# Kernel optimization log

Hardware: AMD Instinct MI355X
Metric: run time of the kernel (lower is better)

The kernel has to match this reference:

```python
import jax, jax.numpy as jnp
import numpy as np

B, N, NB, E, H, A, K, D = 32, 512, 10, 1024, 256, 82, 4, 3


def setup_inputs() -> dict:
    key = jax.random.key(0)
    ks = iter(jax.random.split(key, 64))
    f = lambda shape: jax.random.normal(next(ks), shape, jnp.float32) * 0.05
    inp = {
        "atom_fea": jax.random.normal(next(ks), (B, N, A), jnp.float32),
        "bond_fea": jax.random.normal(next(ks), (B, E, 6), jnp.float32),
        "d_anb": jax.random.randint(next(ks), (B, N, NB), 0, N),
        "d_bnb": jax.random.randint(next(ks), (B, N, NB), 0, E),
        "d_nbs_mask": (jax.random.uniform(next(ks), (B, N, NB)) < 0.8).astype(jnp.float32),
        "d_mask": (jax.random.uniform(next(ks), (B, N)) < 0.9).astype(jnp.float32),
        "Wv": f((A, H)), "bv": f((H,)),
        "Wa_main": f((D, K, H, H)), "ba_main": f((D, K, H)),
        "Wa_super": f((D, K, H, H)), "ba_super": f((D, K, H)),
        "Wm": f((D, K, H, H)), "bm": f((D, K, H)),
        "Wbmm": f((D, K, H)), "bbmm": f((D, K)),
        "Wm2s": f((D, K * H, H)), "bm2s": f((D, H)),
        "Ws2m": f((D, H, H)), "bs2m": f((D, H)),
        "Wsup": f((D, H, H)), "bsup": f((D, H)),
        "Wzm1": f((D, H, H)), "bzm1": f((D, H)),
        "Wzm2": f((D, H, H)), "bzm2": f((D, H)),
        "Wzs1": f((D, H, H)), "bzs1": f((D, H)),
        "Wzs2": f((D, H, H)), "bzs2": f((D, H)),
        "Wu2": f((D, H + 6, H)), "bu2": f((D, H)),
        "Wu1": f((D, 2 * H, H)), "bu1": f((D, H)),
    }
    return inp


def mask_softmax(a, mask):
    a_max = jnp.max(a, -1, keepdims=True)
    e = jnp.exp(a - a_max) * mask
    return e / (jnp.sum(e, -1, keepdims=True) + 1e-6)


def _forward(atom_fea, bond_fea, d_nbs_mask, d_mask,
             Wv, bv, Wa_main, ba_main, Wa_super, ba_super, Wm, bm, Wbmm, bbmm,
             Wm2s, bm2s, Ws2m, bs2m, Wsup, bsup,
             Wzm1, bzm1, Wzm2, bzm2, Wzs1, bzs1, Wzs2, bzs2,
             Wu2, bu2, Wu1, bu1, d_anb, d_bnb):
    Bn = atom_fea.shape[0]
    bidx = jnp.arange(Bn)[:, None, None]
    # vertex embedding (default leaky_relu slope 0.01)
    vf = jax.nn.leaky_relu(atom_fea @ Wv + bv, 0.01)            # [B,N,H]
    sf = jnp.sum(vf * d_mask[:, :, None], axis=1, keepdims=True)  # [B,1,H]
    mask3 = d_nbs_mask[..., None]                               # [B,N,NB,1]
    for d in range(D):
        # --- multi-head main->super attention (vectorized over heads k) ---
        a_main = jnp.tanh(jnp.einsum('bnh,khj->bknj', vf, Wa_main[d]) + ba_main[d][None, :, None, :])
        a_super = jnp.tanh(jnp.einsum('boh,khj->bkoj', sf, Wa_super[d]) + ba_super[d][None, :, None, :])
        a = jnp.einsum('bknh,kh->bkn', a_main * a_super, Wbmm[d]) + bbmm[d][None, :, None]
        attn = mask_softmax(a, d_mask[:, None, :])               # [B,K,N]
        mvf = jnp.einsum('bnh,khj->bknj', vf, Wm[d]) + bm[d][None, :, None, :]
        m2s = jnp.einsum('bkn,bknh->bkh', attn, mvf).reshape(Bn, 1, K * H)
        main_to_super = jnp.tanh(m2s @ Wm2s[d] + bm2s[d])        # [B,1,H]
        # --- wln unit: gather neighbors, MLP, masked sum (slope 0.1) ---
        vnei = vf[bidx, d_anb]                                   # [B,N,NB,H]
        enei = bond_fea[bidx, d_bnb]                             # [B,N,NB,6]
        lnei = jnp.concatenate([vnei, enei], -1)                 # [B,N,NB,H+6]
        nei = jax.nn.leaky_relu(lnei @ Wu2[d] + bu2[d], 0.1)
        nei = jnp.sum(nei * mask3, axis=2)                       # [B,N,H]
        main_self = jax.nn.leaky_relu(jnp.concatenate([vf, nei], -1) @ Wu1[d] + bu1[d], 0.1)
        # --- GRU-style gated updates ---
        super_to_main = jnp.tanh(sf @ Ws2m[d] + bs2m[d])         # [B,1,H]
        super_self = jnp.tanh(sf @ Wsup[d] + bsup[d])            # [B,1,H]
        z_main = jax.nn.sigmoid(main_self @ Wzm1[d] + bzm1[d] + super_to_main @ Wzm2[d] + bzm2[d])
        vf = (1 - z_main) * main_self + z_main * super_to_main
        z_sup = jax.nn.sigmoid(super_self @ Wzs1[d] + bzs1[d] + main_to_super @ Wzs2[d] + bzs2[d])
        sf = (1 - z_sup) * super_self + z_sup * main_to_super    # [B,1,H]; sum over dim 1 is a no-op
    return vf, sf


def reference(atom_fea, bond_fea, d_anb, d_bnb, d_nbs_mask, d_mask,
              Wv, bv, Wa_main, ba_main, Wa_super, ba_super, Wm, bm, Wbmm, bbmm,
              Wm2s, bm2s, Ws2m, bs2m, Wsup, bsup,
              Wzm1, bzm1, Wzm2, bzm2, Wzs1, bzs1, Wzs2, bzs2,
              Wu2, bu2, Wu1, bu1):
    return _forward(atom_fea, bond_fea, d_nbs_mask, d_mask,
                    Wv, bv, Wa_main, ba_main, Wa_super, ba_super, Wm, bm, Wbmm, bbmm,
                    Wm2s, bm2s, Ws2m, bs2m, Wsup, bsup,
                    Wzm1, bzm1, Wzm2, bzm2, Wzs1, bzs1, Wzs2, bzs2,
                    Wu2, bu2, Wu1, bu1, d_anb, d_bnb)
```

## Files before the change

### kernel.cpp

```cpp
#include <hip/hip_runtime.h>
#include <hip/hip_bf16.h>

#define B_ 32
#define N_ 512
#define NB_ 10
#define E_ 1024
#define H_ 256
#define A_ 82
#define K_ 4
#define D_ 3
#define M_ (B_*N_)

typedef unsigned short u16;
typedef __attribute__((ext_vector_type(8))) short bf16x8;
typedef __attribute__((ext_vector_type(4))) float f32x4;

__device__ __forceinline__ float b2f(u16 u){
    unsigned int x = ((unsigned int)u) << 16;
    return __builtin_bit_cast(float, x);
}
__device__ __forceinline__ u16 f2b(float f){
    unsigned int x = __builtin_bit_cast(unsigned int, f);
    unsigned int lsb = (x >> 16) & 1u;
    x += 0x7fffu + lsb;
    return (u16)(x >> 16);
}
__device__ __forceinline__ float sigmoidf_(float x){ return 1.f/(1.f+expf(-x)); }

static constexpr int CVT_N[31] = {
    B_*E_*6, B_*N_*NB_, B_*N_,
    A_*H_, H_,
    D_*K_*H_*H_, D_*K_*H_, D_*K_*H_*H_, D_*K_*H_,
    D_*K_*H_*H_, D_*K_*H_, D_*K_*H_, D_*K_,
    D_*K_*H_*H_, D_*H_, D_*H_*H_, D_*H_,
    D_*H_*H_, D_*H_, D_*H_*H_, D_*H_,
    D_*H_*H_, D_*H_, D_*H_*H_, D_*H_,
    D_*H_*H_, D_*H_, D_*(H_+6)*H_, D_*H_,
    D_*2*H_*H_, D_*H_
};
struct Offs { long v[32]; };
static constexpr Offs mk_offs(){
    Offs o{}; o.v[0]=0;
    for(int i=0;i<31;i++) o.v[i+1]=o.v[i]+CVT_N[i];
    return o;
}
static constexpr Offs CVT_OFF = mk_offs();

struct Ptrs { const void* p[31]; };

__global__ void k_detect(const unsigned short* __restrict__ wv_raw, int* __restrict__ flag){
    float v = b2f(wv_raw[threadIdx.x]);
    bool plaus = (v==v) && (fabsf(v) < 100.0f);
    unsigned long long m = __ballot(plaus);
    if (threadIdx.x==0) *flag = (m == ~0ULL) ? 1 : 0;
}

__global__ void k_cvt(Ptrs ptrs, float* __restrict__ dst, const int* __restrict__ flag){
    int t = blockIdx.y;
    int n = CVT_N[t];
    int i4 = blockIdx.x*256 + threadIdx.x;
    if (i4*4 >= n) return;
    const void* src = ptrs.p[t];
    float4 o;
    if (*flag){
        ushort4 u = ((const ushort4*)src)[i4];
        o.x=b2f(u.x); o.y=b2f(u.y); o.z=b2f(u.z); o.w=b2f(u.w);
    } else {
        o = ((const float4*)src)[i4];
    }
    *(float4*)(dst + CVT_OFF.v[t] + (size_t)i4*4) = o;
}

__global__ void k_wt(const float* __restrict__ Wam, const float* __restrict__ Wu2,
                     const float* __restrict__ Wu1, const float* __restrict__ Wzm1,
                     u16* __restrict__ WT){
    int mi = blockIdx.z;
    const float* src;
    if (mi<12)      src = Wam  + (size_t)mi*H_*H_;
    else if (mi<15) src = Wu2  + (size_t)(mi-12)*(H_+6)*H_;
    else if (mi<18) src = Wu1  + (size_t)(mi-15)*2*H_*H_;
    else if (mi<21) src = Wu1  + (size_t)(mi-18)*2*H_*H_ + (size_t)H_*H_;
    else            src = Wzm1 + (size_t)(mi-21)*H_*H_;
    __shared__ float t[32][33];
    int x = threadIdx.x, y = threadIdx.y;
    int k0 = blockIdx.y*32, n0 = blockIdx.x*32;
    for(int yy=y; yy<32; yy+=8) t[yy][x] = src[(size_t)(k0+yy)*H_ + n0+x];
    __syncthreads();
    u16* dst = WT + ((size_t)mi*8 + (k0>>5))*(256*32);
    for(int yy=y; yy<32; yy+=8) dst[(size_t)(n0+yy)*32 + x] = f2b(t[x][yy]);
}

__global__ void k_embed(const u16* __restrict__ atom, const float* __restrict__ Wv,
                        const float* __restrict__ bv, float* __restrict__ vf,
                        u16* __restrict__ vf_bf, const int* __restrict__ flag){
    __shared__ float arow[8][A_];
    int r0 = blockIdx.x*8; int j = threadIdx.x;
    int fl = *flag;
    for(int i=j;i<8*A_;i+=256){
        int r=i/A_, a=i-r*A_;
        arow[r][a] = fl ? b2f(atom[(size_t)(r0+r)*A_+a])
                        : ((const float*)atom)[(size_t)(r0+r)*A_+a];
    }
    __syncthreads();
    float acc[8];
    float bj = bv[j];
    #pragma unroll
    for(int r=0;r<8;r++) acc[r]=bj;
    for(int a=0;a<A_;a++){
        float w = Wv[a*H_+j];
        #pragma unroll
        for(int r=0;r<8;r++) acc[r] += arow[r][a]*w;
    }
    #pragma unroll
    for(int r=0;r<8;r++){
        float v = acc[r];
        v = v>0.f ? v : 0.01f*v;
        vf[(size_t)(r0+r)*H_+j] = v;
        vf_bf[(size_t)(r0+r)*H_+j] = f2b(v);
    }
}

__global__ void k_sf0(const float* __restrict__ vf, const float* __restrict__ dmask,
                      float* __restrict__ sf){
    int b = blockIdx.x, h = threadIdx.x;
    __shared__ float mk[N_];
    for(int n=threadIdx.x;n<N_;n+=256) mk[n] = dmask[b*N_+n];
    __syncthreads();
    float s=0.f;
    #pragma unroll 8
    for(int n=0;n<N_;n++) s += mk[n]*vf[((size_t)b*N_+n)*H_ + h];
    sf[b*H_+h]=s;
}

__global__ void k_s1(int d, const float* __restrict__ sf,
    const float* __restrict__ Was, const float* __restrict__ bas,
    const float* __restrict__ Wbmm,
    const float* __restrict__ Ws2m, const float* __restrict__ bs2m,
    const float* __restrict__ Wsup, const float* __restrict__ bsup,
    float* __restrict__ asw, float* __restrict__ s2m, float* __restrict__ ssf)
{
    int b = blockIdx.x, m = blockIdx.y, j = threadIdx.x;
    __shared__ float sfl[H_];
    sfl[j] = sf[b*H_+j];
    __syncthreads();
    const float* W; float bias;
    if (m < 4){ W = Was + (size_t)(d*K_+m)*H_*H_; bias = bas[(d*K_+m)*H_+j]; }
    else if (m==4){ W = Ws2m + (size_t)d*H_*H_; bias = bs2m[d*H_+j]; }
    else { W = Wsup + (size_t)d*H_*H_; bias = bsup[d*H_+j]; }
    float acc = bias;
    #pragma unroll 8
    for(int h=0;h<H_;h++) acc += sfl[h]*W[h*H_+j];
    float v = tanhf(acc);
    if (m < 4) asw[(b*K_+m)*H_+j] = v * Wbmm[(d*K_+m)*H_+j];
    else if (m==4) s2m[b*H_+j] = v;
    else ssf[b*H_+j] = v;
}

__global__ void k_s2(int d, const float* __restrict__ s2m,
    const float* __restrict__ Wzm2, const float* __restrict__ bzm2,
    float* __restrict__ stm2p)
{
    int b=blockIdx.x, c=blockIdx.y, j=threadIdx.x;
    __shared__ float xl[64];
    if (j<64) xl[j] = s2m[b*H_ + c*64 + j];
    __syncthreads();
    const float* W = Wzm2 + (size_t)d*H_*H_ + (size_t)(c*64)*H_;
    float acc = (c==0) ? bzm2[d*H_+j] : 0.f;
    #pragma unroll 8
    for(int h=0;h<64;h++) acc += xl[h]*W[h*H_+j];
    stm2p[((size_t)c*B_+b)*H_+j] = acc;
}

__device__ __forceinline__ void gemm_rf(const u16* __restrict__ Abf,
                                        const u16* __restrict__ WTg,
                                        f32x4 acc[2][8])
{
    int tid = threadIdx.x;
    int lane = tid & 63, wave = tid >> 6;
    int wy = wave >> 1, wx = wave & 1;
    int quad = lane >> 4, l15 = lane & 15;
    const u16* aP0 = Abf + (size_t)(wy*32 + l15)*H_ + quad*8;
    const u16* aP1 = aP0 + 16*H_;
    const u16* wP  = WTg + (size_t)(wx*128 + l15)*32 + quad*8;
    #pragma unroll
    for(int mt=0;mt<2;mt++)
        #pragma unroll
        for(int nt=0;nt<8;nt++) acc[mt][nt]=(f32x4){0.f,0.f,0.f,0.f};
    bf16x8 a0[2],a1[2],w0[8],w1[8];
    a0[0]=*(const bf16x8*)(aP0); a0[1]=*(const bf16x8*)(aP1);
    #pragma unroll
    for(int nt=0;nt<8;nt++) w0[nt]=*(const bf16x8*)(wP + nt*512);

#define GLOAD(AN,WN,K0) \
    AN[0]=*(const bf16x8*)(aP0 + (K0)); AN[1]=*(const bf16x8*)(aP1 + (K0)); \
    _Pragma("unroll") for(int nt=0;nt<8;nt++) WN[nt]=*(const bf16x8*)(wP + (size_t)((K0)>>5)*8192 + nt*512);
#define GMMA(AC,WC) \
    _Pragma("unroll") for(int mt=0;mt<2;mt++) \
    _Pragma("unroll") for(int nt=0;nt<8;nt++) \
        acc[mt][nt]=__builtin_amdgcn_mfma_f32_16x16x32_bf16(AC[mt],WC[nt],acc[mt][nt],0,0,0);

    GLOAD(a1,w1,32);  GMMA(a0,w0);
    GLOAD(a0,w0,64);  GMMA(a1,w1);
    GLOAD(a1,w1,96);  GMMA(a0,w0);
    GLOAD(a0,w0,128); GMMA(a1,w1);
    GLOAD(a1,w1,160); GMMA(a0,w0);
    GLOAD(a0,w0,192); GMMA(a1,w1);
    GLOAD(a1,w1,224); GMMA(a0,w0);
    GMMA(a1,w1);
#undef GLOAD
#undef GMMA
}

__global__ __launch_bounds__(256,3) void k_gemm_big(int d, const u16* __restrict__ vf_bf,
    const u16* __restrict__ WT, const float* __restrict__ ba_main,
    const float* __restrict__ bbmm, const float* __restrict__ bu1,
    const float* __restrict__ asw, float* __restrict__ score,
    float* __restrict__ proj_u2, float* __restrict__ pu1a)
{
    __shared__ float sred[64*33];
    int m0 = blockIdx.x*64;
    int seg = blockIdx.y;
    int b = m0 >> 9;
    int mi;
    if (seg < 4)      mi = d*4+seg;
    else if (seg==4)  mi = 12+d;
    else              mi = 15+d;
    f32x4 acc[2][8];
    gemm_rf(vf_bf + (size_t)m0*H_, WT + (size_t)mi*H_*H_, acc);
    int tid=threadIdx.x, lane=tid&63, wave=tid>>6;
    int wy=wave>>1, wx=wave&1, quad=lane>>4, l15=lane&15;
    if (seg < 4){
        const float* aswp = asw + (size_t)(b*K_+seg)*H_;
        const float* bap  = ba_main + (size_t)(d*K_+seg)*H_;
        float bbv[8], awv[8];
        #pragma unroll
        for(int nt=0;nt<8;nt++){
            int col = wx*128+nt*16+l15;
            bbv[nt]=bap[col]; awv[nt]=aswp[col];
        }
        #pragma unroll
        for(int mt=0;mt<2;mt++)
            #pragma unroll
            for(int r=0;r<4;r++){
                float p=0.f;
                #pragma unroll
                for(int nt=0;nt<8;nt++)
                    p += tanhf(acc[mt][nt][r]+bbv[nt])*awv[nt];
                int row = wy*32+mt*16+quad*4+r;
                sred[row*33 + wx*16+l15] = p;
            }
        __syncthreads();
        if (tid < 64){
            float s=0.f;
            #pragma unroll 8
            for(int i=0;i<32;i++) s += sred[tid*33+i];
            score[(size_t)(b*K_+seg)*N_ + (m0&511) + tid] = s + bbmm[d*K_+seg];
        }
    } else if (seg==4){
        #pragma unroll
        for(int mt=0;mt<2;mt++)
            #pragma unroll
            for(int nt=0;nt<8;nt++){
                int col = wx*128+nt*16+l15;
                #pragma unroll
                for(int r=0;r<4;r++){
                    int row = m0 + wy*32+mt*16+quad*4+r;
                    proj_u2[(size_t)row*H_+col] = acc[mt][nt][r];
                }
            }
    } else {
        const float* bp = bu1 + d*H_;
        #pragma unroll
        for(int mt=0;mt<2;mt++)
            #pragma unroll
            for(int nt=0;nt<8;nt++){
                int col = wx*128+nt*16+l15;
                float bb = bp[col];
                #pragma unroll
                for(int r=0;r<4;r++){
                    int row = m0 + wy*32+mt*16+quad*4+r;
                    pu1a[(size_t)row*H_+col] = acc[mt][nt][r] + bb;
                }
            }
    }
}

__global__ __launch_bounds__(256,3) void k_mainself(int d, u16* __restrict__ neims,
    const u16* __restrict__ WT, float* __restrict__ pu)
{
    int m0 = blockIdx.x*64;
    f32x4 acc[2][8];
    gemm_rf(neims + (size_t)m0*H_, WT + (size_t)(18+d)*H_*H_, acc);
    __syncthreads();
    int tid=threadIdx.x, lane=tid&63, wave=tid>>6;
    int wy=wave>>1, wx=wave&1, quad=lane>>4, l15=lane&15;
    #pragma unroll
    for(int mt=0;mt<2;mt++)
        #pragma unroll
        for(int nt=0;nt<8;nt++){
            int col = wx*128+nt*16+l15;
            #pragma unroll
            for(int r=0;r<4;r++){
                int row = m0 + wy*32+mt*16+quad*4+r;
                float v = acc[mt][nt][r] + pu[(size_t)row*H_+col];
                v = v>0.f? v : 0.1f*v;
                pu[(size_t)row*H_+col] = v;
                neims[(size_t)row*H_+col] = f2b(v);
            }
        }
}

__global__ __launch_bounds__(256,3) void k_update(int d, const float* __restrict__ ms,
    const u16* __restrict__ ms_bf, const u16* __restrict__ WT, const float* __restrict__ bzm1,
    const float* __restrict__ stm2p, const float* __restrict__ s2m,
    float* __restrict__ vf, u16* __restrict__ vf_bf)
{
    int m0 = blockIdx.x*64; int b = m0>>9;
    f32x4 acc[2][8];
    gemm_rf(ms_bf + (size_t)m0*H_, WT + (size_t)(21+d)*H_*H_, acc);
    int tid=threadIdx.x, lane=tid&63, wave=tid>>6;
    int wy=wave>>1, wx=wave&1, quad=lane>>4, l15=lane&15;
    #pragma unroll
    for(int mt=0;mt<2;mt++)
        #pragma unroll
        for(int nt=0;nt<8;nt++){
            int col = wx*128+nt*16+l15;
            float bz = bzm1[d*H_+col];
            float st = stm2p[(size_t)(0*B_+b)*H_+col] + stm2p[(size_t)(1*B_+b)*H_+col]
                     + stm2p[(size_t)(2*B_+b)*H_+col] + stm2p[(size_t)(3*B_+b)*H_+col];
            float sm = s2m[b*H_+col];
            #pragma unroll
            for(int r=0;r<4;r++){
                int row = m0 + wy*32+mt*16+quad*4+r;
                float z = sigmoidf_(acc[mt][nt][r] + bz + st);
                float msv = ms[(size_t)row*H_+col];
                float o = (1.f-z)*msv + z*sm;
                vf[(size_t)row*H_+col] = o;
                vf_bf[(size_t)row*H_+col] = f2b(o);
            }
        }
}

__global__ void k_softmax(float* __restrict__ score, const float* __restrict__ dmask,
                          float* __restrict__ sumattn){
    int b = blockIdx.x, k = blockIdx.y;
    int tid = threadIdx.x;
    __shared__ float sh[256];
    float* a = score + (size_t)(b*K_+k)*N_;
    float v0 = a[tid], v1 = a[tid+256];
    sh[tid]=fmaxf(v0,v1); __syncthreads();
    for(int s=128;s>0;s>>=1){ if(tid<s) sh[tid]=fmaxf(sh[tid],sh[tid+s]); __syncthreads(); }
    float m = sh[0]; __syncthreads();
    float e0 = expf(v0-m)*dmask[b*N_+tid], e1 = expf(v1-m)*dmask[b*N_+tid+256];
    sh[tid]=e0+e1; __syncthreads();
    for(int s=128;s>0;s>>=1){ if(tid<s) sh[tid]+=sh[tid+s]; __syncthreads(); }
    float S = sh[0];
    float inv = 1.f/(S+1e-6f);
    a[tid]=e0*inv; a[tid+256]=e1*inv;
    if(tid==0) sumattn[b*K_+k]=S*inv;
}

__global__ void k_t2(const float* __restrict__ attn, const float* __restrict__ vf,
                     float* __restrict__ tpart){
    int b=blockIdx.x, k=blockIdx.y, c=blockIdx.z, h=threadIdx.x;
    __shared__ float at[256];
    at[h] = attn[(size_t)(b*K_+k)*N_ + c*256 + h];
    __syncthreads();
    float acc=0.f;
    const float* vfp = vf + ((size_t)b*N_ + c*256)*H_ + h;
    #pragma unroll 8
    for(int n=0;n<256;n++) acc += at[n]*vfp[(size_t)n*H_];
    tpart[((size_t)(c*B_+b)*K_+k)*H_+h]=acc;
}

__global__ void k_m1(int d, const float* __restrict__ tpart, const float* __restrict__ sumattn,
    const float* __restrict__ Wm, const float* __restrict__ bm, float* __restrict__ m2s)
{
    int b=blockIdx.x, k=blockIdx.y, j=threadIdx.x;
    __shared__ float tl[H_];
    tl[j] = tpart[((size_t)(0*B_+b)*K_+k)*H_+j] + tpart[((size_t)(1*B_+b)*K_+k)*H_+j];
    __syncthreads();
    const float* W = Wm + (size_t)(d*K_+k)*H_*H_;
    float acc = sumattn[b*K_+k]*bm[(d*K_+k)*H_+j];
    #pragma unroll 8
    for(int h=0;h<H_;h++) acc += tl[h]*W[h*H_+j];
    m2s[(size_t)(b*K_+k)*H_+j]=acc;
}

__global__ void k_m2(int d, const float* __restrict__ m2s, const float* __restrict__ Wm2s,
                     float* __restrict__ mtsp)
{
    int b=blockIdx.x, c=blockIdx.y, j=threadIdx.x;
    __shared__ float xl[H_];
    xl[j]=m2s[(size_t)(b*K_+c)*H_+j];
    __syncthreads();
    const float* W = Wm2s + (size_t)d*(K_*H_)*H_ + (size_t)(c*H_)*H_;
    float acc=0.f;
    #pragma unroll 8
    for(int h=0;h<H_;h++) acc += xl[h]*W[h*H_+j];
    mtsp[((size_t)c*B_+b)*H_+j]=acc;
}

__global__ void k_mts(int d, const float* __restrict__ mtsp, const float* __restrict__ bm2s,
                      float* __restrict__ mts){
    int b=blockIdx.x, j=threadIdx.x;
    float acc = bm2s[d*H_+j];
    #pragma unroll
    for(int c=0;c<4;c++) acc += mtsp[((size_t)c*B_+b)*H_+j];
    mts[b*H_+j]=tanhf(acc);
}

__global__ void k_m3(int d, const float* __restrict__ ssf, const float* __restrict__ mts,
    const float* __restrict__ Wzs1, const float* __restrict__ Wzs2,
    float* __restrict__ p1, float* __restrict__ p2)
{
    int b=blockIdx.x, m=blockIdx.y, j=threadIdx.x;
    __shared__ float xl[H_];
    const float* x = m ? mts : ssf;
    xl[j]=x[b*H_+j];
    __syncthreads();
    const float* W = (m ? Wzs2 : Wzs1) + (size_t)d*H_*H_;
    float acc=0.f;
    #pragma unroll 8
    for(int h=0;h<H_;h++) acc += xl[h]*W[h*H_+j];
    (m ? p2 : p1)[b*H_+j]=acc;
}

__global__ void k_sfup(int d, const float* __restrict__ p1, const float* __restrict__ p2,
    const float* __restrict__ bzs1, const float* __restrict__ bzs2,
    const float* __restrict__ ssf, const float* __restrict__ mts, float* __restrict__ sf)
{
    int b=blockIdx.x, j=threadIdx.x;
    float z = sigmoidf_(p1[b*H_+j]+bzs1[d*H_+j]+p2[b*H_+j]+bzs2[d*H_+j]);
    sf[b*H_+j]=(1.f-z)*ssf[b*H_+j]+z*mts[b*H_+j];
}

__global__ void k_nei(int d, const int* __restrict__ anb, const int* __restrict__ bnb,
    const float* __restrict__ nbm, const float* __restrict__ bond,
    const float* __restrict__ Wu2, const float* __restrict__ bu2,
    const float* __restrict__ proj_u2, u16* __restrict__ nei_bf)
{
    __shared__ float W2s[6][256];
    __shared__ float bfeat[4][NB_][6];
    __shared__ int ai[4][NB_]; __shared__ int bi[4][NB_]; __shared__ float mk[4][NB_];
    int r0 = blockIdx.x*4; int b = r0 >> 9; int h = threadIdx.x;
    const float* W2 = Wu2 + (size_t)d*(H_+6)*H_ + (size_t)H_*H_;
    for(int i=h;i<6*H_;i+=256) W2s[i>>8][i&255] = W2[i];
    if (h < 4*NB_){
        int r=h/NB_, jn=h-r*NB_;
        ai[r][jn]=anb[(size_t)(r0+r)*NB_+jn];
        bi[r][jn]=bnb[(size_t)(r0+r)*NB_+jn];
        mk[r][jn]=nbm[(size_t)(r0+r)*NB_+jn];
    }
    __syncthreads();
    if (h < 4*NB_*6){
        int r=h/(NB_*6), rem=h-r*(NB_*6), jn=rem/6, i=rem-jn*6;
        bfeat[r][jn][i]=bond[((size_t)b*E_+bi[r][jn])*6+i];
    }
    __syncthreads();
    float bu = bu2[d*H_+h];
    #pragma unroll
    for(int r=0;r<4;r++){
        float acc=0.f;
        #pragma unroll
        for(int jn=0;jn<NB_;jn++){
            float v = proj_u2[((size_t)b*N_+ai[r][jn])*H_+h] + bu;
            #pragma unroll
            for(int i=0;i<6;i++) v += bfeat[r][jn][i]*W2s[i][h];
            v = v>0.f? v : 0.1f*v;
            acc += mk[r][jn]*v;
        }
        nei_bf[(size_t)(r0+r)*H_+h]=f2b(acc);
    }
}

__global__ void k_out(const float* __restrict__ vf, const float* __restrict__ sf,
                      void* __restrict__ out, const int* __restrict__ flag){
    int idx = blockIdx.x*256 + threadIdx.x;
    const int total = M_*H_ + B_*H_;
    if (idx >= total) return;
    float v = (idx < M_*H_) ? vf[idx] : sf[idx - M_*H_];
    if (*flag) ((unsigned short*)out)[idx] = f2b(v);
    else       ((float*)out)[idx] = v;
}

extern "C" void kernel_launch(void* const* d_in, const int* in_sizes, int n_in,
                              void* d_out, int out_size, void* d_ws, size_t ws_size,
                              hipStream_t stream)
{
    const int* anb = (const int*)d_in[2];
    const int* bnb = (const int*)d_in[3];

    float* ws   = (float*)d_ws;
    int*   flag = (int*)ws;
    float* cvt  = ws + 64;
    float* p    = cvt + ((CVT_OFF.v[31] + 63) & ~63L);
    float* vf        = p; p += (size_t)M_*H_;
    float* proj_u2   = p; p += (size_t)M_*H_;
    float* proj_u1a  = p; p += (size_t)M_*H_;
    u16*   vf_bf     = (u16*)p; p += (size_t)M_*H_/2;
    u16*   neims     = (u16*)p; p += (size_t)M_*H_/2;
    float* sf        = p; p += B_*H_;
    float* score     = p; p += B_*K_*N_;
    float* sumattn   = p; p += B_*K_;
    float* asw       = p; p += B_*K_*H_;
    float* s2m       = p; p += B_*H_;
    float* ssf       = p; p += B_*H_;
    float* stm2p     = p; p += 4*B_*H_;
    float* tpart     = p; p += 2*B_*K_*H_;
    float* m2s       = p; p += B_*K_*H_;
    float* mtsp      = p; p += 4*B_*H_;
    float* mts       = p; p += B_*H_;
    float* p1        = p; p += B_*H_;
    float* p2        = p; p += B_*H_;
    u16*   WT        = (u16*)p;

    const float* cBond = cvt + CVT_OFF.v[0];
    const float* cNbm  = cvt + CVT_OFF.v[1];
    const float* cDm   = cvt + CVT_OFF.v[2];
    const float* cWv   = cvt + CVT_OFF.v[3];
    const float* cbv   = cvt + CVT_OFF.v[4];
    const float* cWam  = cvt + CVT_OFF.v[5];
    const float* cbam  = cvt + CVT_OFF.v[6];
    const float* cWas  = cvt + CVT_OFF.v[7];
    const float* cbas  = cvt + CVT_OFF.v[8];
    const float* cWm   = cvt + CVT_OFF.v[9];
    const float* cbm   = cvt + CVT_OFF.v[10];
    const float* cWbmm = cvt + CVT_OFF.v[11];
    const float* cbbmm = cvt + CVT_OFF.v[12];
    const float* cWm2s = cvt + CVT_OFF.v[13];
    const float* cbm2s = cvt + CVT_OFF.v[14];
    const float* cWs2m = cvt + CVT_OFF.v[15];
    const float* cbs2m = cvt + CVT_OFF.v[16];
    const float* cWsup = cvt + CVT_OFF.v[17];
    const float* cbsup = cvt + CVT_OFF.v[18];
    const float* cWzm1 = cvt + CVT_OFF.v[19];
    const float* cbzm1 = cvt + CVT_OFF.v[20];
    const float* cWzm2 = cvt + CVT_OFF.v[21];
    const float* cbzm2 = cvt + CVT_OFF.v[22];
    const float* cWzs1 = cvt + CVT_OFF.v[23];
    const float* cbzs1 = cvt + CVT_OFF.v[24];
    const float* cWzs2 = cvt + CVT_OFF.v[25];
    const float* cbzs2 = cvt + CVT_OFF.v[26];
    const float* cWu2  = cvt + CVT_OFF.v[27];
    const float* cbu2  = cvt + CVT_OFF.v[28];
    const float* cWu1  = cvt + CVT_OFF.v[29];
    const float* cbu1  = cvt + CVT_OFF.v[30];

    Ptrs ptrs;
    {
        int idx[31] = {1,4,5,6,7,8,9,10,11,12,13,14,15,16,17,18,19,20,21,
                       22,23,24,25,26,27,28,29,30,31,32,33};
        for(int i=0;i<31;i++) ptrs.p[i] = d_in[idx[i]];
    }

    k_detect<<<1,64,0,stream>>>((const unsigned short*)d_in[6], flag);
    {
        int maxv4 = (D_*K_*H_*H_ + 3)/4;
        int gx = (maxv4 + 255)/256;
        k_cvt<<<dim3(gx,31),256,0,stream>>>(ptrs, cvt, flag);
    }
    k_wt<<<dim3(8,8,24),dim3(32,8),0,stream>>>(cWam, cWu2, cWu1, cWzm1, WT);

    k_embed<<<M_/8,256,0,stream>>>((const u16*)d_in[0], cWv, cbv, vf, vf_bf, flag);
    k_sf0<<<B_,256,0,stream>>>(vf, cDm, sf);
    for(int d=0; d<D_; d++){
        k_s1<<<dim3(B_,6),256,0,stream>>>(d, sf, cWas, cbas, cWbmm,
                                          cWs2m, cbs2m, cWsup, cbsup, asw, s2m, ssf);
        k_s2<<<dim3(B_,4),256,0,stream>>>(d, s2m, cWzm2, cbzm2, stm2p);
        k_gemm_big<<<dim3(M_/64,6),256,0,stream>>>(d, vf_bf, WT, cbam, cbbmm, cbu1,
                                                   asw, score, proj_u2, proj_u1a);
        k_softmax<<<dim3(B_,K_),256,0,stream>>>(score, cDm, sumattn);
        k_t2<<<dim3(B_,K_,2),256,0,stream>>>(score, vf, tpart);
        k_m1<<<dim3(B_,K_),256,0,stream>>>(d, tpart, sumattn, cWm, cbm, m2s);
        k_m2<<<dim3(B_,4),256,0,stream>>>(d, m2s, cWm2s, mtsp);
        k_mts<<<B_,256,0,stream>>>(d, mtsp, cbm2s, mts);
        k_m3<<<dim3(B_,2),256,0,stream>>>(d, ssf, mts, cWzs1, cWzs2, p1, p2);
        k_sfup<<<B_,256,0,stream>>>(d, p1, p2, cbzs1, cbzs2, ssf, mts, sf);
        k_nei<<<M_/4,256,0,stream>>>(d, anb, bnb, cNbm, cBond, cWu2, cbu2, proj_u2, neims);
        k_mainself<<<M_/64,256,0,stream>>>(d, neims, WT, proj_u1a);
        k_update<<<M_/64,256,0,stream>>>(d, proj_u1a, neims, WT, cbzm1, stm2p, s2m, vf, vf_bf);
    }
    k_out<<<(M_*H_+B_*H_+255)/256,256,0,stream>>>(vf, sf, d_out, flag);
}
```

Before: 766.4 us.

## Stage weight tiles into LDS via async global_load_lds double buffering

Before, each wave loaded its weight fragments straight from global memory into registers. Now each 32-wide K slice of the weight matrix is staged into a double-buffered LDS tile with global_load_lds, and the weight transpose kernel writes a fragment-ordered layout that matches this. The aim is to share weight loads across the four waves of a block and overlap the next slice's fetch with the current MFMAs. In exchange it adds a barrier per K step and 32KB of LDS per block, which may cut occupancy below the launch-bounds target of 3 blocks.

After: 725.4 us. -5.3%, faster.

```diff
diff --git a/kernel.cpp b/kernel.cpp
--- a/kernel.cpp
+++ b/kernel.cpp
@@ -86,8 +86,12 @@
     int k0 = blockIdx.y*32, n0 = blockIdx.x*32;
     for(int yy=y; yy<32; yy+=8) t[yy][x] = src[(size_t)(k0+yy)*H_ + n0+x];
     __syncthreads();
-    u16* dst = WT + ((size_t)mi*8 + (k0>>5))*(256*32);
-    for(int yy=y; yy<32; yy+=8) dst[(size_t)(n0+yy)*32 + x] = f2b(t[x][yy]);
+    u16* dst = WT + ((size_t)mi*8 + (k0>>5))*8192;
+    int quad = x>>3, j = x&7;
+    for(int yy=y; yy<32; yy+=8){
+        int n = n0+yy, nt = n>>4, lv = n&15;
+        dst[nt*512 + quad*128 + lv*8 + j] = f2b(t[x][yy]);
+    }
 }
 
 __global__ void k_embed(const u16* __restrict__ atom, const float* __restrict__ Wv,
@@ -171,9 +175,21 @@
     stm2p[((size_t)c*B_+b)*H_+j] = acc;
 }
 
-__device__ __forceinline__ void gemm_rf(const u16* __restrict__ Abf,
-                                        const u16* __restrict__ WTg,
-                                        f32x4 acc[2][8])
+__device__ __forceinline__ void stageW(const u16* __restrict__ g, u16* l){
+    int t = threadIdx.x;
+    const u16* gs = g + t*8;
+    u16* ls = l + t*8;
+    #pragma unroll
+    for(int it=0; it<4; ++it)
+        __builtin_amdgcn_global_load_lds(
+            (const __attribute__((address_space(1))) void*)(gs + it*2048),
+            (__attribute__((address_space(3))) void*)(ls + it*2048),
+            16, 0, 0);
+}
+
+__device__ __forceinline__ void gemm_ldsW(const u16* __restrict__ Abf,
+                                          const u16* __restrict__ WTg,
+                                          u16* Wlds, f32x4 acc[2][8])
 {
     int tid = threadIdx.x;
     int lane = tid & 63, wave = tid >> 6;
@@ -181,34 +197,38 @@
     int quad = lane >> 4, l15 = lane & 15;
     const u16* aP0 = Abf + (size_t)(wy*32 + l15)*H_ + quad*8;
     const u16* aP1 = aP0 + 16*H_;
-    const u16* wP  = WTg + (size_t)(wx*128 + l15)*32 + quad*8;
+    bf16x8 a[4][2];
+    #pragma unroll
+    for(int s=0;s<3;s++){
+        a[s][0] = *(const bf16x8*)(aP0 + s*32);
+        a[s][1] = *(const bf16x8*)(aP1 + s*32);
+    }
+    stageW(WTg, Wlds);
     #pragma unroll
     for(int mt=0;mt<2;mt++)
         #pragma unroll
         for(int nt=0;nt<8;nt++) acc[mt][nt]=(f32x4){0.f,0.f,0.f,0.f};
-    bf16x8 a0[2],a1[2],w0[8],w1[8];
-    a0[0]=*(const bf16x8*)(aP0); a0[1]=*(const bf16x8*)(aP1);
-    #pragma unroll
-    for(int nt=0;nt<8;nt++) w0[nt]=*(const bf16x8*)(wP + nt*512);
-
-#define GLOAD(AN,WN,K0) \
-    AN[0]=*(const bf16x8*)(aP0 + (K0)); AN[1]=*(const bf16x8*)(aP1 + (K0)); \
-    _Pragma("unroll") for(int nt=0;nt<8;nt++) WN[nt]=*(const bf16x8*)(wP + (size_t)((K0)>>5)*8192 + nt*512);
-#define GMMA(AC,WC) \
-    _Pragma("unroll") for(int mt=0;mt<2;mt++) \
-    _Pragma("unroll") for(int nt=0;nt<8;nt++) \
-        acc[mt][nt]=__builtin_amdgcn_mfma_f32_16x16x32_bf16(AC[mt],WC[nt],acc[mt][nt],0,0,0);
-
-    GLOAD(a1,w1,32);  GMMA(a0,w0);
-    GLOAD(a0,w0,64);  GMMA(a1,w1);
-    GLOAD(a1,w1,96);  GMMA(a0,w0);
-    GLOAD(a0,w0,128); GMMA(a1,w1);
-    GLOAD(a1,w1,160); GMMA(a0,w0);
-    GLOAD(a0,w0,192); GMMA(a1,w1);
-    GLOAD(a1,w1,224); GMMA(a0,w0);
-    GMMA(a1,w1);
-#undef GLOAD
-#undef GMMA
+    __syncthreads();
+    #pragma unroll
+    for(int s=0;s<8;s++){
+        if (s<7) stageW(WTg + (size_t)(s+1)*8192, Wlds + ((s+1)&1)*8192);
+        if (s<5){
+            int sl = s+3;
+            a[sl&3][0] = *(const bf16x8*)(aP0 + sl*32);
+            a[sl&3][1] = *(const bf16x8*)(aP1 + sl*32);
+        }
+        const u16* wb = Wlds + (s&1)*8192 + wx*4096 + quad*128 + l15*8;
+        bf16x8 w[8];
+        #pragma unroll
+        for(int nt=0;nt<8;nt++) w[nt] = *(const bf16x8*)(wb + nt*512);
+        #pragma unroll
+        for(int mt=0;mt<2;mt++)
+            #pragma unroll
+            for(int nt=0;nt<8;nt++)
+                acc[mt][nt] = __builtin_amdgcn_mfma_f32_16x16x32_bf16(
+                    a[s&3][mt], w[nt], acc[mt][nt], 0,0,0);
+        __syncthreads();
+    }
 }
 
 __global__ __launch_bounds__(256,3) void k_gemm_big(int d, const u16* __restrict__ vf_bf,
@@ -217,7 +237,7 @@
     const float* __restrict__ asw, float* __restrict__ score,
     float* __restrict__ proj_u2, float* __restrict__ pu1a)
 {
-    __shared__ float sred[64*33];
+    __shared__ __attribute__((aligned(16))) u16 Wlds[2*8192];
     int m0 = blockIdx.x*64;
     int seg = blockIdx.y;
     int b = m0 >> 9;
@@ -226,10 +246,11 @@
     else if (seg==4)  mi = 12+d;
     else              mi = 15+d;
     f32x4 acc[2][8];
-    gemm_rf(vf_bf + (size_t)m0*H_, WT + (size_t)mi*H_*H_, acc);
+    gemm_ldsW(vf_bf + (size_t)m0*H_, WT + (size_t)mi*H_*H_, Wlds, acc);
     int tid=threadIdx.x, lane=tid&63, wave=tid>>6;
     int wy=wave>>1, wx=wave&1, quad=lane>>4, l15=lane&15;
     if (seg < 4){
+        float* sred = (float*)Wlds;
         const float* aswp = asw + (size_t)(b*K_+seg)*H_;
         const float* bap  = ba_main + (size_t)(d*K_+seg)*H_;
         float bbv[8], awv[8];
@@ -288,10 +309,10 @@
 __global__ __launch_bounds__(256,3) void k_mainself(int d, u16* __restrict__ neims,
     const u16* __restrict__ WT, float* __restrict__ pu)
 {
+    __shared__ __attribute__((aligned(16))) u16 Wlds[2*8192];
     int m0 = blockIdx.x*64;
     f32x4 acc[2][8];
-    gemm_rf(neims + (size_t)m0*H_, WT + (size_t)(18+d)*H_*H_, acc);
-    __syncthreads();
+    gemm_ldsW(neims + (size_t)m0*H_, WT + (size_t)(18+d)*H_*H_, Wlds, acc);
     int tid=threadIdx.x, lane=tid&63, wave=tid>>6;
     int wy=wave>>1, wx=wave&1, quad=lane>>4, l15=lane&15;
     #pragma unroll
@@ -315,9 +336,10 @@
     const float* __restrict__ stm2p, const float* __restrict__ s2m,
     float* __restrict__ vf, u16* __restrict__ vf_bf)
 {
+    __shared__ __attribute__((aligned(16))) u16 Wlds[2*8192];
     int m0 = blockIdx.x*64; int b = m0>>9;
     f32x4 acc[2][8];
-    gemm_rf(ms_bf + (size_t)m0*H_, WT + (size_t)(21+d)*H_*H_, acc);
+    gemm_ldsW(ms_bf + (size_t)m0*H_, WT + (size_t)(21+d)*H_*H_, Wlds, acc);
     int tid=threadIdx.x, lane=tid&63, wave=tid>>6;
     int wy=wave>>1, wx=wave&1, quad=lane>>4, l15=lane&15;
     #pragma unroll
```
